# Kernel optimization log

Hardware: AMD Instinct MI355X
Metric: run time of the kernel (lower is better)

Reference implementation:

```python
import jax, jax.numpy as jnp
import numpy as np

N, D, K = 32768, 256, 2048
BETA = 0.25  # init arg beta, in [0,1) branch of the loss


def setup_inputs() -> dict:
    key = jax.random.key(0)
    k1, k2 = jax.random.split(key)
    x = jax.random.normal(k1, (N, D), dtype=jnp.float32)
    # mimics nn.Embedding init: uniform(-1/K, 1/K) then mean-centered
    cb = jax.random.uniform(k2, (K, D), dtype=jnp.float32, minval=-1.0 / K, maxval=1.0 / K)
    codebook = cb - cb.mean(axis=0)
    return {"x": x, "codebook": codebook}


def reference(x, codebook):
    # pairwise squared L2 distances: [N, K]
    dist = (
        jnp.sum(x * x, axis=1, keepdims=True)
        + jnp.sum(codebook * codebook, axis=1)
        - 2.0 * jnp.matmul(x, codebook.T)
    )
    encoding_inds = jnp.argmin(dist, axis=1)  # [N]
    # one-hot @ codebook == gather of nearest code vectors
    x_codebook = jnp.take(codebook, encoding_inds, axis=0)  # [N, D]
    # straight-through quantization
    x_quantized = x + jax.lax.stop_gradient(x_codebook - x)
    # VQ loss, beta in [0, 1) branch
    commit = jnp.mean((x - jax.lax.stop_gradient(x_codebook)) ** 2)
    embed = jnp.mean((x_codebook - jax.lax.stop_gradient(x)) ** 2)
    loss = BETA * commit + embed
    return x_quantized, loss
```

## Files before the change

kernel.cpp:

```cpp
#include <hip/hip_runtime.h>

#define N_ROWS 32768
#define DIM    256
#define KCODES 2048
#define CSCALE 4096.0f
#define BROWS  32

typedef __attribute__((ext_vector_type(16))) float f32x16;
typedef __attribute__((ext_vector_type(4)))  unsigned int u32x4;

union frag16 { u32x4 v; long l[2]; };

__device__ __forceinline__ uint4 pack16(const float* s) {
    int a = __builtin_amdgcn_cvt_pk_fp8_f32(s[0],  s[1],  0, false);
    a     = __builtin_amdgcn_cvt_pk_fp8_f32(s[2],  s[3],  a, true);
    int b = __builtin_amdgcn_cvt_pk_fp8_f32(s[4],  s[5],  0, false);
    b     = __builtin_amdgcn_cvt_pk_fp8_f32(s[6],  s[7],  b, true);
    int c = __builtin_amdgcn_cvt_pk_fp8_f32(s[8],  s[9],  0, false);
    c     = __builtin_amdgcn_cvt_pk_fp8_f32(s[10], s[11], c, true);
    int d = __builtin_amdgcn_cvt_pk_fp8_f32(s[12], s[13], 0, false);
    d     = __builtin_amdgcn_cvt_pk_fp8_f32(s[14], s[15], d, true);
    uint4 o; o.x = a; o.y = b; o.z = c; o.w = d;
    return o;
}

__global__ void prep_h(const float* __restrict__ cb,
                       float* __restrict__ halfcn, float* __restrict__ loss) {
    const int t    = threadIdx.x;
    const int code = blockIdx.x * 4 + (t >> 6);
    const int s    = t & 63;
    if (blockIdx.x == 0 && t == 0) *loss = 0.0f;
    const int kc = s >> 4, d = (s >> 2) & 3, b4 = (s & 3) * 4;
    const int h = d >> 1, q = d & 1;
    const int k0 = kc * 64 + q * 32 + (b4 >> 3) * 16 + h * 8 + (b4 & 7);
    float4 v = *(const float4*)&cb[(size_t)code * DIM + k0];
    float ssum = v.x * v.x + v.y * v.y + v.z * v.z + v.w * v.w;
    #pragma unroll
    for (int o = 32; o > 0; o >>= 1) ssum += __shfl_down(ssum, o, 64);
    if (s == 0) halfcn[code] = 0.5f * CSCALE * ssum;
}

__global__ void prep_frag(const float* __restrict__ cb, uint4* __restrict__ cbF) {
    const int gid = blockIdx.x * 256 + threadIdx.x;
    const int L   = gid & 63;
    const int r   = gid >> 6;
    const int j   = r & 1;
    const int ct  = (r >> 1) & 1;
    const int w   = (r >> 2) & 3;
    const int i   = r >> 4;
    const int pass = i >> 2, kc = i & 3;
    const int h   = L >> 5, l32 = L & 31;
    const int code = pass * 256 + w * 64 + ct * 32 + l32;
    float buf[16];
    #pragma unroll
    for (int b = 0; b < 4; b++) {
        const int k0 = kc * 64 + j * 32 + (b >> 1) * 16 + h * 8 + (b & 1) * 4;
        float4 v = *(const float4*)&cb[(size_t)code * DIM + k0];
        buf[b * 4 + 0] = v.x * CSCALE; buf[b * 4 + 1] = v.y * CSCALE;
        buf[b * 4 + 2] = v.z * CSCALE; buf[b * 4 + 3] = v.w * CSCALE;
    }
    cbF[gid] = pack16(buf);
}

__global__ __launch_bounds__(256, 3) void vq_fused(
        const float* __restrict__ x, const float* __restrict__ cb,
        const uint4* __restrict__ cbF, const float* __restrict__ halfcn,
        float* __restrict__ out, float* __restrict__ loss) {
    __shared__ char As[4][2048];
    __shared__ float hcs[KCODES];
    struct Tail { float red[BROWS][4]; int idxs[BROWS]; float lred[4]; };
    Tail* tl = (Tail*)As;

    const int t    = threadIdx.x;
    const int lane = t & 63;
    const int w    = t >> 6;
    const int l32  = lane & 31;
    const int h    = lane >> 5;
    const int row0 = blockIdx.x * BROWS;

    {
        const int r   = t >> 3;
        const int kc  = (t >> 1) & 3;
        const int pp  = t & 1;
        const int key = (r >> 1) & 3;
        const float* src = x + (size_t)(row0 + r) * DIM + kc * 64;
        float buf[16];
        #pragma unroll
        for (int pi = 0; pi < 2; pi++) {
            const int p = pp * 2 + pi;
            const int d = p ^ key, hh = d >> 1, qq = d & 1;
            #pragma unroll
            for (int j = 0; j < 4; j++) *(float4*)(buf + j * 4) =
                *(const float4*)(src + qq * 32 + (j >> 1) * 16 + hh * 8 + (j & 1) * 4);
            *(uint4*)(As[kc] + r * 64 + p * 16) = pack16(buf);
        }
        #pragma unroll
        for (int jj = 0; jj < 8; jj++) hcs[jj * 256 + t] = halfcn[jj * 256 + t];
    }

    const int key = (l32 >> 1) & 3;
    const int p0  = (h * 2 + 0) ^ key;
    const int p1  = (h * 2 + 1) ^ key;

    float mp[16];
    #pragma unroll
    for (int r = 0; r < 16; r++) mp[r] = -3.0e38f;

    const char* bbase = (const char*)cbF + w * 4096 + (size_t)lane * 16;

    frag16 bfr[3][4];
    #pragma unroll
    for (int s = 0; s < 3; s++)
        #pragma unroll
        for (int c = 0; c < 4; c++)
            bfr[s][c].v = *(const u32x4*)(bbase + s * 16384 + c * 1024);

    __syncthreads();

    frag16 afr[4][2];
    #pragma unroll
    for (int kc = 0; kc < 4; kc++) {
        const char* ab = As[kc];
        const int rbase = l32 * 64;
        afr[kc][0].v = *(const u32x4*)(ab + rbase + p0 * 16);
        afr[kc][1].v = *(const u32x4*)(ab + rbase + p1 * 16);
    }

    #pragma unroll
    for (int pass = 0; pass < 8; ++pass) {
        const float hc0 = hcs[pass * 256 + w * 64 + l32];
        const float hc1 = hcs[pass * 256 + w * 64 + 32 + l32];
        f32x16 acc[2];
        #pragma unroll
        for (int r = 0; r < 16; r++) {
            acc[0][r] = -hc0;
            acc[1][r] = -hc1;
        }

        #pragma unroll
        for (int kc = 0; kc < 4; ++kc) {
            const int i  = pass * 4 + kc;
            const int sl = i % 3;

            frag16 cur[4];
            #pragma unroll
            for (int c = 0; c < 4; c++) cur[c] = bfr[sl][c];

            if (i + 3 < 32) {
                #pragma unroll
                for (int c = 0; c < 4; c++)
                    bfr[sl][c].v = *(const u32x4*)(bbase + (i + 3) * 16384 + c * 1024);
            }

            #pragma unroll
            for (int q = 0; q < 2; q++)
                #pragma unroll
                for (int hf = 0; hf < 2; hf++)
                    #pragma unroll
                    for (int ct = 0; ct < 2; ct++)
                        acc[ct] = __builtin_amdgcn_mfma_f32_32x32x16_fp8_fp8(
                            afr[kc][q].l[hf], cur[ct * 2 + q].l[hf],
                            acc[ct], 0, 0, 0);
        }

        #pragma unroll
        for (int ct = 0; ct < 2; ct++) {
            const unsigned code = (unsigned)(pass * 256 + w * 64 + ct * 32 + l32);
            #pragma unroll
            for (int r = 0; r < 16; r++) {
                unsigned u = (__float_as_uint(acc[ct][r]) & 0xFFFFF800u) | code;
                mp[r] = fmaxf(mp[r], __uint_as_float(u));
            }
        }
    }

    #pragma unroll
    for (int m = 1; m <= 16; m <<= 1)
        #pragma unroll
        for (int r = 0; r < 16; r++)
            mp[r] = fmaxf(mp[r], __shfl_xor(mp[r], m, 64));

    __syncthreads();

    if (l32 == 0) {
        #pragma unroll
        for (int r = 0; r < 16; r++) {
            const int row = (r & 3) + 8 * (r >> 2) + 4 * h;
            tl->red[row][w] = mp[r];
        }
    }
    __syncthreads();
    if (t < BROWS) {
        float b0 = fmaxf(fmaxf(tl->red[t][0], tl->red[t][1]),
                         fmaxf(tl->red[t][2], tl->red[t][3]));
        tl->idxs[t] = (int)(__float_as_uint(b0) & 2047u);
    }
    __syncthreads();

    float lsum = 0.0f;
    #pragma unroll 4
    for (int r = 0; r < BROWS; r++) {
        const int code = tl->idxs[r];
        const float c  = cb[(size_t)code * DIM + t];
        const float xv = x[(size_t)(row0 + r) * DIM + t];
        out[(size_t)(row0 + r) * DIM + t] = c;
        const float d = xv - c;
        lsum += d * d;
    }
    #pragma unroll
    for (int o = 32; o > 0; o >>= 1) lsum += __shfl_down(lsum, o, 64);
    if (lane == 0) tl->lred[w] = lsum;
    __syncthreads();
    if (t == 0) {
        const float scale = 1.25f / (float)((size_t)N_ROWS * DIM);
        atomicAdd(loss, (tl->lred[0] + tl->lred[1] + tl->lred[2] + tl->lred[3]) * scale);
    }
}

extern "C" void kernel_launch(void* const* d_in, const int* in_sizes, int n_in,
                              void* d_out, int out_size, void* d_ws, size_t ws_size,
                              hipStream_t stream) {
    const float* x  = (const float*)d_in[0];
    const float* cb = (const float*)d_in[1];
    float* out  = (float*)d_out;
    float* loss = out + (size_t)N_ROWS * DIM;

    char* ws = (char*)d_ws;
    uint4* cbF    = (uint4*)ws;
    float* halfcn = (float*)(ws + (size_t)KCODES * 256);

    prep_h   <<<KCODES / 4, 256, 0, stream>>>(cb, halfcn, loss);
    prep_frag<<<128,        256, 0, stream>>>(cb, cbF);
    vq_fused <<<N_ROWS / BROWS, 256, 0, stream>>>(x, cb, cbF, halfcn, out, loss);
}
```

Before: 123.2 us.

## Double rows per block and split waves into 2x2 row/code groups

```diff
diff --git a/kernel.cpp b/kernel.cpp
--- a/kernel.cpp
+++ b/kernel.cpp
@@ -4,7 +4,7 @@
 #define DIM    256
 #define KCODES 2048
 #define CSCALE 4096.0f
-#define BROWS  32
+#define BROWS  64
 
 typedef __attribute__((ext_vector_type(16))) float f32x16;
 typedef __attribute__((ext_vector_type(4)))  unsigned int u32x4;
@@ -41,16 +41,16 @@
 }
 
 __global__ void prep_frag(const float* __restrict__ cb, uint4* __restrict__ cbF) {
-    const int gid = blockIdx.x * 256 + threadIdx.x;
-    const int L   = gid & 63;
-    const int r   = gid >> 6;
-    const int j   = r & 1;
-    const int ct  = (r >> 1) & 1;
-    const int w   = (r >> 2) & 3;
-    const int i   = r >> 4;
-    const int pass = i >> 2, kc = i & 3;
-    const int h   = L >> 5, l32 = L & 31;
-    const int code = pass * 256 + w * 64 + ct * 32 + l32;
+    const int gid  = blockIdx.x * 256 + threadIdx.x;
+    const int L    = gid & 63;
+    const int rest = gid >> 6;
+    const int j    = rest & 1;
+    const int ct   = (rest >> 1) & 1;
+    const int cg   = (rest >> 2) & 1;
+    const int i    = rest >> 3;
+    const int p    = i >> 2, kc = i & 3;
+    const int h    = L >> 5, l32 = L & 31;
+    const int code = p * 128 + cg * 64 + ct * 32 + l32;
     float buf[16];
     #pragma unroll
     for (int b = 0; b < 4; b++) {
@@ -66,9 +66,9 @@
         const float* __restrict__ x, const float* __restrict__ cb,
         const uint4* __restrict__ cbF, const float* __restrict__ halfcn,
         float* __restrict__ out, float* __restrict__ loss) {
-    __shared__ char As[4][2048];
+    __shared__ char As[4][4096];
     __shared__ float hcs[KCODES];
-    struct Tail { float red[BROWS][4]; int idxs[BROWS]; float lred[4]; };
+    struct Tail { float red[BROWS][2]; int idxs[BROWS]; float lred[4]; };
     Tail* tl = (Tail*)As;
 
     const int t    = threadIdx.x;
@@ -77,17 +77,17 @@
     const int l32  = lane & 31;
     const int h    = lane >> 5;
     const int row0 = blockIdx.x * BROWS;
+    const int wrow = (w >> 1) * 32;
+    const int cg   = w & 1;
 
     {
-        const int r   = t >> 3;
-        const int kc  = (t >> 1) & 3;
-        const int pp  = t & 1;
+        const int r   = t >> 2;
+        const int kc  = t & 3;
         const int key = (r >> 1) & 3;
         const float* src = x + (size_t)(row0 + r) * DIM + kc * 64;
         float buf[16];
         #pragma unroll
-        for (int pi = 0; pi < 2; pi++) {
-            const int p = pp * 2 + pi;
+        for (int p = 0; p < 4; p++) {
             const int d = p ^ key, hh = d >> 1, qq = d & 1;
             #pragma unroll
             for (int j = 0; j < 4; j++) *(float4*)(buf + j * 4) =
@@ -106,14 +106,14 @@
     #pragma unroll
     for (int r = 0; r < 16; r++) mp[r] = -3.0e38f;
 
-    const char* bbase = (const char*)cbF + w * 4096 + (size_t)lane * 16;
+    const char* bbase = (const char*)cbF + cg * 4096 + (size_t)lane * 16;
 
     frag16 bfr[3][4];
     #pragma unroll
     for (int s = 0; s < 3; s++)
         #pragma unroll
         for (int c = 0; c < 4; c++)
-            bfr[s][c].v = *(const u32x4*)(bbase + s * 16384 + c * 1024);
+            bfr[s][c].v = *(const u32x4*)(bbase + s * 8192 + c * 1024);
 
     __syncthreads();
 
@@ -121,15 +121,15 @@
     #pragma unroll
     for (int kc = 0; kc < 4; kc++) {
         const char* ab = As[kc];
-        const int rbase = l32 * 64;
+        const int rbase = (wrow + l32) * 64;
         afr[kc][0].v = *(const u32x4*)(ab + rbase + p0 * 16);
         afr[kc][1].v = *(const u32x4*)(ab + rbase + p1 * 16);
     }
 
     #pragma unroll
-    for (int pass = 0; pass < 8; ++pass) {
-        const float hc0 = hcs[pass * 256 + w * 64 + l32];
-        const float hc1 = hcs[pass * 256 + w * 64 + 32 + l32];
+    for (int pass = 0; pass < 16; ++pass) {
+        const float hc0 = hcs[pass * 128 + cg * 64 + l32];
+        const float hc1 = hcs[pass * 128 + cg * 64 + 32 + l32];
         f32x16 acc[2];
         #pragma unroll
         for (int r = 0; r < 16; r++) {
@@ -146,10 +146,10 @@
             #pragma unroll
             for (int c = 0; c < 4; c++) cur[c] = bfr[sl][c];
 
-            if (i + 3 < 32) {
+            if (i + 3 < 64) {
                 #pragma unroll
                 for (int c = 0; c < 4; c++)
-                    bfr[sl][c].v = *(const u32x4*)(bbase + (i + 3) * 16384 + c * 1024);
+                    bfr[sl][c].v = *(const u32x4*)(bbase + (i + 3) * 8192 + c * 1024);
             }
 
             #pragma unroll
@@ -165,7 +165,7 @@
 
         #pragma unroll
         for (int ct = 0; ct < 2; ct++) {
-            const unsigned code = (unsigned)(pass * 256 + w * 64 + ct * 32 + l32);
+            const unsigned code = (unsigned)(pass * 128 + cg * 64 + ct * 32 + l32);
             #pragma unroll
             for (int r = 0; r < 16; r++) {
                 unsigned u = (__float_as_uint(acc[ct][r]) & 0xFFFFF800u) | code;
@@ -185,14 +185,13 @@
     if (l32 == 0) {
         #pragma unroll
         for (int r = 0; r < 16; r++) {
-            const int row = (r & 3) + 8 * (r >> 2) + 4 * h;
-            tl->red[row][w] = mp[r];
+            const int row = wrow + (r & 3) + 8 * (r >> 2) + 4 * h;
+            tl->red[row][cg] = mp[r];
         }
     }
     __syncthreads();
     if (t < BROWS) {
-        float b0 = fmaxf(fmaxf(tl->red[t][0], tl->red[t][1]),
-                         fmaxf(tl->red[t][2], tl->red[t][3]));
+        float b0 = fmaxf(tl->red[t][0], tl->red[t][1]);
         tl->idxs[t] = (int)(__float_as_uint(b0) & 2047u);
     }
     __syncthreads();
```

Result: no change. 122.3 us (-0.7%).
